# Kernel optimization log

Measured on AMD Instinct MI355X. Metric: run time of the kernel, lower is better.

Reference implementation:

```python
import jax, jax.numpy as jnp
import numpy as np

N = 100_000      # nodes
E = 1_600_000    # edges
DIN = 128
DH = 128
DOUT = 2
BN_EPS = 1e-5


def setup_inputs() -> dict:
    key = jax.random.key(0)
    ks = jax.random.split(key, 14)
    s_in = 1.0 / np.sqrt(DIN)
    s_h = 1.0 / np.sqrt(DH)
    return {
        "x": jax.random.normal(ks[0], (N, DIN), jnp.float32),
        "edge_index": jax.random.randint(ks[1], (2, E), 0, N, jnp.int32),
        "W1": jax.random.normal(ks[2], (DIN, DH), jnp.float32) * s_in,
        "b1": jnp.zeros((DH,), jnp.float32),
        "W2": jax.random.normal(ks[3], (DH, DH), jnp.float32) * s_h,
        "b2": jnp.zeros((DH,), jnp.float32),
        "W3": jax.random.normal(ks[4], (DH, DH), jnp.float32) * s_h,
        "b3": jnp.zeros((DH,), jnp.float32),
        "gamma": jnp.ones((DH,), jnp.float32),
        "beta": jnp.zeros((DH,), jnp.float32),
        "Wc": jax.random.normal(ks[5], (DH, DH), jnp.float32) * s_h,
        "bc": jnp.zeros((DH,), jnp.float32),
        "Wr": jax.random.normal(ks[6], (DH, DOUT), jnp.float32) * s_h,
        "br": jnp.zeros((DOUT,), jnp.float32),
    }


def reference(x, edge_index, W1, b1, W2, b2, W3, b3, gamma, beta, Wc, bc, Wr, br):
    src, dst = edge_index[0], edge_index[1]
    # GCN symmetric normalization with self-loops (deg includes self-loop)
    deg = jnp.zeros((N,), x.dtype).at[dst].add(1.0) + 1.0
    dinv = jax.lax.rsqrt(deg)
    coef = (dinv[src] * dinv[dst])[:, None]        # [E,1]
    self_coef = (dinv * dinv)[:, None]             # [N,1] self-loop weight

    def gcn_conv(h, W, b):
        h = h @ W                                  # [N,DH] dense transform
        agg = jnp.zeros((N, h.shape[1]), h.dtype).at[dst].add(h[src] * coef)
        return agg + h * self_coef + b

    h = jax.nn.relu(gcn_conv(x, W1, b1))
    h = jax.nn.relu(gcn_conv(h, W2, b2))   # dropout is identity at inference
    h = jax.nn.relu(gcn_conv(h, W3, b3))
    # BatchNorm1d over the node dimension (training-mode batch statistics)
    mu = h.mean(axis=0)
    var = h.var(axis=0)
    h = (h - mu) * jax.lax.rsqrt(var + BN_EPS) * gamma + beta
    h = jax.nn.relu(h @ Wc + bc)
    return h @ Wr + br
```

## Files before the change

### kernel.cpp

```cpp
#include <hip/hip_runtime.h>

#define DHC 128
#define BSHIFT 8
#define BSIZE 256

typedef __attribute__((ext_vector_type(8))) __bf16 bf16x8;
typedef __attribute__((ext_vector_type(8))) unsigned short ushort8;
typedef __attribute__((ext_vector_type(4))) float floatx4;

__device__ inline unsigned short f2bf(float f) {
    unsigned int u = __float_as_uint(f);
    return (unsigned short)((u + 0x7FFFu + ((u >> 16) & 1u)) >> 16);
}
__device__ inline float bf2f_lo(unsigned int v) { return __uint_as_float(v << 16); }
__device__ inline float bf2f_hi(unsigned int v) { return __uint_as_float(v & 0xFFFF0000u); }


__global__ __launch_bounds__(256) void bucket_hist(const int* __restrict__ dst,
                                                   int* __restrict__ bcount, int e) {
    __shared__ int h[512];
    for (int i = threadIdx.x; i < 512; i += 256) h[i] = 0;
    __syncthreads();
    int base = blockIdx.x * 4096 + threadIdx.x;
#pragma unroll
    for (int j = 0; j < 16; j++) {
        int i = base + j * 256;
        if (i < e) atomicAdd(&h[dst[i] >> BSHIFT], 1);
    }
    __syncthreads();
    for (int i = threadIdx.x; i < 512; i += 256)
        if (h[i]) atomicAdd(&bcount[i], h[i]);
}

__global__ void bucket_scan(const int* __restrict__ bcount, int* __restrict__ bbase,
                            int* __restrict__ bcur, int* __restrict__ row_ptr,
                            int nb, int n, int e) {
    __shared__ int s[512];
    int t = threadIdx.x;
    s[t] = (t < nb) ? bcount[t] : 0;
    __syncthreads();
    for (int off = 1; off < 512; off <<= 1) {
        int add = (t >= off) ? s[t - off] : 0;
        __syncthreads();
        s[t] += add;
        __syncthreads();
    }
    if (t < nb) {
        int ex = (t == 0) ? 0 : s[t - 1];
        bbase[t] = ex;
        bcur[t] = ex;
    }
    if (t == 0) {
        bbase[nb] = e;
        row_ptr[n] = e;
    }
}

__global__ __launch_bounds__(256) void bucket_scatter(const int* __restrict__ src,
                                                      const int* __restrict__ dst,
                                                      int* __restrict__ bcur,
                                                      unsigned int* __restrict__ ebuf, int e) {
    __shared__ int h[512];
    __shared__ int rsv[512];
    for (int i = threadIdx.x; i < 512; i += 256) h[i] = 0;
    __syncthreads();
    int base = blockIdx.x * 4096 + threadIdx.x;
    int sreg[16], dreg[16];
#pragma unroll
    for (int j = 0; j < 16; j++) {
        int i = base + j * 256;
        if (i < e) {
            sreg[j] = src[i];
            dreg[j] = dst[i];
            atomicAdd(&h[dreg[j] >> BSHIFT], 1);
        } else {
            dreg[j] = -1;
        }
    }
    __syncthreads();
    for (int i = threadIdx.x; i < 512; i += 256) {
        int c = h[i];
        rsv[i] = c ? atomicAdd(&bcur[i], c) : 0;
        h[i] = 0;
    }
    __syncthreads();
#pragma unroll
    for (int j = 0; j < 16; j++) {
        if (dreg[j] >= 0) {
            int b = dreg[j] >> BSHIFT;
            int pos = rsv[b] + atomicAdd(&h[b], 1);
            ebuf[pos] = (unsigned int)sreg[j] | ((unsigned int)(dreg[j] & (BSIZE - 1)) << 20);
        }
    }
}

__global__ __launch_bounds__(256) void bucket_build(const unsigned int* __restrict__ ebuf,
                                                    const int* __restrict__ bbase,
                                                    int* __restrict__ row_ptr,
                                                    int* __restrict__ csr_src,
                                                    float* __restrict__ dinv,
                                                    float* __restrict__ selfc, int n) {
    __shared__ int ldeg[256];
    __shared__ int lcur[256];
    int b = blockIdx.x;
    int t = threadIdx.x;
    int beg = bbase[b], end = bbase[b + 1];
    ldeg[t] = 0;
    __syncthreads();
    for (int i = beg + t; i < end; i += 256) atomicAdd(&ldeg[ebuf[i] >> 20], 1);
    __syncthreads();
    int deg = ldeg[t];
    lcur[t] = deg;
    __syncthreads();
    for (int off = 1; off < 256; off <<= 1) {
        int add = (t >= off) ? lcur[t - off] : 0;
        __syncthreads();
        lcur[t] += add;
        __syncthreads();
    }
    int rp = beg + lcur[t] - deg;
    int node = (b << BSHIFT) + t;
    if (node < n) {
        row_ptr[node] = rp;
        float dv = rsqrtf((float)(deg + 1));
        dinv[node] = dv;
        selfc[node] = dv * dv;
    }
    __syncthreads();
    lcur[t] = rp;
    __syncthreads();
    for (int i = beg + t; i < end; i += 256) {
        unsigned int p = ebuf[i];
        int pos = atomicAdd(&lcur[p >> 20], 1);
        csr_src[pos] = (int)(p & 0xFFFFFu);
    }
}

__global__ void wconv3_k(const float* __restrict__ W1, const float* __restrict__ W2,
                         const float* __restrict__ W3, unsigned short* __restrict__ WTall) {
    int idx = blockIdx.x * 256 + threadIdx.x;
    int wsel = idx >> 14;
    int i = idx & 16383;
    int nn = i >> 7, k = i & 127;
    const float* W = (wsel == 0) ? W1 : (wsel == 1) ? W2 : W3;
    WTall[idx] = f2bf(W[k * 128 + nn]);
}

template <int MODE, int AF32>
__global__ __launch_bounds__(256, 4) void gemm_k(const void* __restrict__ Avoid,
                                                 const unsigned short* __restrict__ WT,
                                                 const float* __restrict__ bias,
                                                 unsigned short* __restrict__ outB,
                                                 float* __restrict__ outF,
                                                 const float* __restrict__ Wr,
                                                 const float* __restrict__ br, int n) {
    __shared__ unsigned short Ws[32 * 512];
    {
        for (int c = threadIdx.x; c < 2048; c += 256) {
            int f = c >> 6;
            int l = c & 63;
            int ks = f >> 3, ct = f & 7;
            int nn = ct * 16 + (l & 15);
            int kb = ks * 32 + (l >> 4) * 8;
            *(uint4*)(&Ws[c * 8]) = *(const uint4*)(&WT[nn * 128 + kb]);
        }
    }
    __syncthreads();
    const int wave = threadIdx.x >> 6;
    const int lane = threadIdx.x & 63;
    const int rowbase = blockIdx.x * 128 + wave * 32;
    const int m = lane & 15;
    const int kq = lane >> 4;

    floatx4 acc[2][8];
#pragma unroll
    for (int rt = 0; rt < 2; rt++)
#pragma unroll
        for (int ct = 0; ct < 8; ct++) acc[rt][ct] = (floatx4){0.f, 0.f, 0.f, 0.f};

    const int r0 = min(rowbase + m, n - 1);
    const int r1 = min(rowbase + 16 + m, n - 1);

#pragma unroll
    for (int ks = 0; ks < 4; ks++) {
        const int kb = ks * 32 + kq * 8;
        bf16x8 a0, a1;
        if (AF32) {
            const float* Af = (const float*)Avoid;
            float4 f00 = *(const float4*)(Af + (size_t)r0 * 128 + kb);
            float4 f01 = *(const float4*)(Af + (size_t)r0 * 128 + kb + 4);
            float4 f10 = *(const float4*)(Af + (size_t)r1 * 128 + kb);
            float4 f11 = *(const float4*)(Af + (size_t)r1 * 128 + kb + 4);
            ushort8 u0, u1;
            u0[0] = f2bf(f00.x); u0[1] = f2bf(f00.y); u0[2] = f2bf(f00.z); u0[3] = f2bf(f00.w);
            u0[4] = f2bf(f01.x); u0[5] = f2bf(f01.y); u0[6] = f2bf(f01.z); u0[7] = f2bf(f01.w);
            u1[0] = f2bf(f10.x); u1[1] = f2bf(f10.y); u1[2] = f2bf(f10.z); u1[3] = f2bf(f10.w);
            u1[4] = f2bf(f11.x); u1[5] = f2bf(f11.y); u1[6] = f2bf(f11.z); u1[7] = f2bf(f11.w);
            a0 = __builtin_bit_cast(bf16x8, u0);
            a1 = __builtin_bit_cast(bf16x8, u1);
        } else {
            const unsigned short* Ab = (const unsigned short*)Avoid;
            a0 = __builtin_bit_cast(bf16x8, *(const ushort8*)(Ab + (size_t)r0 * 128 + kb));
            a1 = __builtin_bit_cast(bf16x8, *(const ushort8*)(Ab + (size_t)r1 * 128 + kb));
        }
#pragma unroll
        for (int ct = 0; ct < 8; ct++) {
            bf16x8 bfr = __builtin_bit_cast(bf16x8,
                *(const ushort8*)(&Ws[(ks * 8 + ct) * 512 + lane * 8]));
            acc[0][ct] = __builtin_amdgcn_mfma_f32_16x16x32_bf16(a0, bfr, acc[0][ct], 0, 0, 0);
            acc[1][ct] = __builtin_amdgcn_mfma_f32_16x16x32_bf16(a1, bfr, acc[1][ct], 0, 0, 0);
        }
    }

    if (MODE == 0) {
#pragma unroll
        for (int rt = 0; rt < 2; rt++) {
#pragma unroll
            for (int ct = 0; ct < 8; ct++) {
                int col = ct * 16 + m;
#pragma unroll
                for (int i = 0; i < 4; i++) {
                    int r = rowbase + rt * 16 + kq * 4 + i;
                    if (r < n) outB[(size_t)r * 128 + col] = f2bf(acc[rt][ct][i]);
                }
            }
        }
    } else {
        float bcv[8], wr0[8], wr1[8];
#pragma unroll
        for (int ct = 0; ct < 8; ct++) {
            int col = ct * 16 + m;
            bcv[ct] = bias[col];
            float2 wv = ((const float2*)Wr)[col];
            wr0[ct] = wv.x;
            wr1[ct] = wv.y;
        }
        float br0 = br[0], br1 = br[1];
#pragma unroll
        for (int rt = 0; rt < 2; rt++) {
#pragma unroll
            for (int i = 0; i < 4; i++) {
                float p0 = 0.f, p1 = 0.f;
#pragma unroll
                for (int ct = 0; ct < 8; ct++) {
                    float v = fmaxf(acc[rt][ct][i] + bcv[ct], 0.f);
                    p0 = fmaf(v, wr0[ct], p0);
                    p1 = fmaf(v, wr1[ct], p1);
                }
#pragma unroll
                for (int mk = 1; mk < 16; mk <<= 1) {
                    p0 += __shfl_xor(p0, mk);
                    p1 += __shfl_xor(p1, mk);
                }
                int r = rowbase + rt * 16 + kq * 4 + i;
                if (m == 0 && r < n) ((float2*)outF)[r] = make_float2(p0 + br0, p1 + br1);
            }
        }
    }
}

__global__ __launch_bounds__(256) void agg_k(const unsigned short* __restrict__ hW,
                                             const int* __restrict__ csr,
                                             const int* __restrict__ row_ptr,
                                             const float* __restrict__ dinv,
                                             const float* __restrict__ selfc,
                                             const float* __restrict__ bias,
                                             unsigned short* __restrict__ out, int n) {
    int node = blockIdx.x * 16 + (threadIdx.x >> 4);
    int t = threadIdx.x & 15;
    if (node >= n) return;
    int beg = row_ptr[node], end = row_ptr[node + 1];
    float dd = dinv[node];
    const uint4* h4 = (const uint4*)hW;
    float a[8];
#pragma unroll
    for (int i = 0; i < 8; i++) a[i] = 0.f;

    int e = beg;
    for (; e + 3 < end; e += 4) {
        int s0 = csr[e + 0], s1 = csr[e + 1], s2 = csr[e + 2], s3 = csr[e + 3];
        float c0 = dinv[s0] * dd, c1 = dinv[s1] * dd, c2 = dinv[s2] * dd, c3 = dinv[s3] * dd;
        uint4 v0 = h4[(size_t)s0 * 16 + t];
        uint4 v1 = h4[(size_t)s1 * 16 + t];
        uint4 v2 = h4[(size_t)s2 * 16 + t];
        uint4 v3 = h4[(size_t)s3 * 16 + t];
        a[0] = fmaf(c0, bf2f_lo(v0.x), a[0]); a[1] = fmaf(c0, bf2f_hi(v0.x), a[1]);
        a[2] = fmaf(c0, bf2f_lo(v0.y), a[2]); a[3] = fmaf(c0, bf2f_hi(v0.y), a[3]);
        a[4] = fmaf(c0, bf2f_lo(v0.z), a[4]); a[5] = fmaf(c0, bf2f_hi(v0.z), a[5]);
        a[6] = fmaf(c0, bf2f_lo(v0.w), a[6]); a[7] = fmaf(c0, bf2f_hi(v0.w), a[7]);
        a[0] = fmaf(c1, bf2f_lo(v1.x), a[0]); a[1] = fmaf(c1, bf2f_hi(v1.x), a[1]);
        a[2] = fmaf(c1, bf2f_lo(v1.y), a[2]); a[3] = fmaf(c1, bf2f_hi(v1.y), a[3]);
        a[4] = fmaf(c1, bf2f_lo(v1.z), a[4]); a[5] = fmaf(c1, bf2f_hi(v1.z), a[5]);
        a[6] = fmaf(c1, bf2f_lo(v1.w), a[6]); a[7] = fmaf(c1, bf2f_hi(v1.w), a[7]);
        a[0] = fmaf(c2, bf2f_lo(v2.x), a[0]); a[1] = fmaf(c2, bf2f_hi(v2.x), a[1]);
        a[2] = fmaf(c2, bf2f_lo(v2.y), a[2]); a[3] = fmaf(c2, bf2f_hi(v2.y), a[3]);
        a[4] = fmaf(c2, bf2f_lo(v2.z), a[4]); a[5] = fmaf(c2, bf2f_hi(v2.z), a[5]);
        a[6] = fmaf(c2, bf2f_lo(v2.w), a[6]); a[7] = fmaf(c2, bf2f_hi(v2.w), a[7]);
        a[0] = fmaf(c3, bf2f_lo(v3.x), a[0]); a[1] = fmaf(c3, bf2f_hi(v3.x), a[1]);
        a[2] = fmaf(c3, bf2f_lo(v3.y), a[2]); a[3] = fmaf(c3, bf2f_hi(v3.y), a[3]);
        a[4] = fmaf(c3, bf2f_lo(v3.z), a[4]); a[5] = fmaf(c3, bf2f_hi(v3.z), a[5]);
        a[6] = fmaf(c3, bf2f_lo(v3.w), a[6]); a[7] = fmaf(c3, bf2f_hi(v3.w), a[7]);
    }
    for (; e < end; e++) {
        int s = csr[e];
        float c = dinv[s] * dd;
        uint4 v = h4[(size_t)s * 16 + t];
        a[0] = fmaf(c, bf2f_lo(v.x), a[0]); a[1] = fmaf(c, bf2f_hi(v.x), a[1]);
        a[2] = fmaf(c, bf2f_lo(v.y), a[2]); a[3] = fmaf(c, bf2f_hi(v.y), a[3]);
        a[4] = fmaf(c, bf2f_lo(v.z), a[4]); a[5] = fmaf(c, bf2f_hi(v.z), a[5]);
        a[6] = fmaf(c, bf2f_lo(v.w), a[6]); a[7] = fmaf(c, bf2f_hi(v.w), a[7]);
    }

    {
        float sc = selfc[node];
        uint4 v = h4[(size_t)node * 16 + t];
        a[0] = fmaf(sc, bf2f_lo(v.x), a[0]); a[1] = fmaf(sc, bf2f_hi(v.x), a[1]);
        a[2] = fmaf(sc, bf2f_lo(v.y), a[2]); a[3] = fmaf(sc, bf2f_hi(v.y), a[3]);
        a[4] = fmaf(sc, bf2f_lo(v.z), a[4]); a[5] = fmaf(sc, bf2f_hi(v.z), a[5]);
        a[6] = fmaf(sc, bf2f_lo(v.w), a[6]); a[7] = fmaf(sc, bf2f_hi(v.w), a[7]);
    }
    float4 b0 = ((const float4*)bias)[t * 2];
    float4 b1 = ((const float4*)bias)[t * 2 + 1];
    uint4 o;
    o.x = (unsigned int)f2bf(fmaxf(a[0] + b0.x, 0.f)) |
          ((unsigned int)f2bf(fmaxf(a[1] + b0.y, 0.f)) << 16);
    o.y = (unsigned int)f2bf(fmaxf(a[2] + b0.z, 0.f)) |
          ((unsigned int)f2bf(fmaxf(a[3] + b0.w, 0.f)) << 16);
    o.z = (unsigned int)f2bf(fmaxf(a[4] + b1.x, 0.f)) |
          ((unsigned int)f2bf(fmaxf(a[5] + b1.y, 0.f)) << 16);
    o.w = (unsigned int)f2bf(fmaxf(a[6] + b1.z, 0.f)) |
          ((unsigned int)f2bf(fmaxf(a[7] + b1.w, 0.f)) << 16);
    ((uint4*)out)[(size_t)node * 16 + t] = o;
}

__global__ __launch_bounds__(256) void bn_stats(const unsigned short* __restrict__ h,
                                                float* __restrict__ gsum,
                                                float* __restrict__ gsumsq, int n) {
    __shared__ float red[4][256];
    int l = threadIdx.x & 63;
    int rs = threadIdx.x >> 6;
    float s0 = 0.f, s1 = 0.f, q0 = 0.f, q1 = 0.f;
    for (int r = blockIdx.x * 4 + rs; r < n; r += gridDim.x * 4) {
        unsigned int v = *(const unsigned int*)(h + (size_t)r * 128 + l * 2);
        float a = bf2f_lo(v), b = bf2f_hi(v);
        s0 += a;
        s1 += b;
        q0 = fmaf(a, a, q0);
        q1 = fmaf(b, b, q1);
    }
    red[0][threadIdx.x] = s0;
    red[1][threadIdx.x] = s1;
    red[2][threadIdx.x] = q0;
    red[3][threadIdx.x] = q1;
    __syncthreads();
    if (threadIdx.x < 64) {
        float S0 = 0.f, S1 = 0.f, Q0 = 0.f, Q1 = 0.f;
#pragma unroll
        for (int j = 0; j < 4; j++) {
            S0 += red[0][j * 64 + l];
            S1 += red[1][j * 64 + l];
            Q0 += red[2][j * 64 + l];
            Q1 += red[3][j * 64 + l];
        }
        atomicAdd(&gsum[2 * l + 0], S0);
        atomicAdd(&gsum[2 * l + 1], S1);
        atomicAdd(&gsumsq[2 * l + 0], Q0);
        atomicAdd(&gsumsq[2 * l + 1], Q1);
    }
}

__global__ void bn_fold(const float* __restrict__ gsum, const float* __restrict__ gsumsq,
                        const float* __restrict__ gamma, const float* __restrict__ beta,
                        const float* __restrict__ Wc, const float* __restrict__ bc,
                        unsigned short* __restrict__ WcT, float* __restrict__ bcP, float invN) {
    __shared__ float scaleS[128], shiftS[128];
    int j = threadIdx.x;
    float mu = gsum[j] * invN;
    float var = gsumsq[j] * invN - mu * mu;
    float sc = gamma[j] * rsqrtf(var + 1e-5f);
    scaleS[j] = sc;
    shiftS[j] = beta[j] - mu * sc;
    __syncthreads();
    float accB = bc[j];
    for (int k = 0; k < 128; k++) {
        float w = Wc[k * 128 + j];
        WcT[j * 128 + k] = f2bf(scaleS[k] * w);
        accB = fmaf(shiftS[k], w, accB);
    }
    bcP[j] = accB;
}


extern "C" void kernel_launch(void* const* d_in, const int* in_sizes, int n_in,
                              void* d_out, int out_size, void* d_ws, size_t ws_size,
                              hipStream_t stream) {
    const float* x = (const float*)d_in[0];
    const int* ei = (const int*)d_in[1];
    const float* W1 = (const float*)d_in[2];
    const float* b1 = (const float*)d_in[3];
    const float* W2 = (const float*)d_in[4];
    const float* b2 = (const float*)d_in[5];
    const float* W3 = (const float*)d_in[6];
    const float* b3 = (const float*)d_in[7];
    const float* gamma = (const float*)d_in[8];
    const float* beta = (const float*)d_in[9];
    const float* Wc = (const float*)d_in[10];
    const float* bc = (const float*)d_in[11];
    const float* Wr = (const float*)d_in[12];
    const float* br = (const float*)d_in[13];
    float* out = (float*)d_out;

    const int N = in_sizes[0] / DHC;
    const int E = in_sizes[1] / 2;
    const int* srcIdx = ei;
    const int* dstIdx = ei + E;
    const int NB = (N + BSIZE - 1) >> BSHIFT;

    char* w = (char*)d_ws;
    size_t off = 0;
    auto alloc = [&](size_t bytes) -> void* {
        void* p = w + off;
        off += (bytes + 255) & ~(size_t)255;
        return p;
    };
    unsigned short* bufA = (unsigned short*)alloc((size_t)N * DHC * 2);
    unsigned short* bufB = (unsigned short*)alloc((size_t)N * DHC * 2);
    unsigned int* ebuf = (unsigned int*)alloc((size_t)E * 4);
    int* csr_src = (int*)alloc((size_t)E * 4);
    int* row_ptr = (int*)alloc((size_t)(N + 1) * 4);
    float* dinv = (float*)alloc((size_t)N * 4);
    float* selfc = (float*)alloc((size_t)N * 4);
    int* bcount = (int*)alloc(512 * 4 + 256 * 4);
    float* stats = (float*)(bcount + 512);
    float* gsum = stats;
    float* gsumsq = stats + 128;
    int* bbase = (int*)alloc(512 * 4);
    int* bcur = (int*)alloc(512 * 4);
    unsigned short* WTall = (unsigned short*)alloc((size_t)3 * 16384 * 2);
    unsigned short* WT1 = WTall;
    unsigned short* WT2 = WTall + 16384;
    unsigned short* WT3 = WTall + 32768;
    unsigned short* WcT = (unsigned short*)alloc(16384 * 2);
    float* bcP = (float*)alloc(128 * 4);
    (void)ws_size; (void)n_in; (void)out_size;

    hipMemsetAsync(bcount, 0, 512 * 4 + 256 * 4, stream);

    const int EB = (E + 4095) / 4096;
    bucket_hist<<<EB, 256, 0, stream>>>(dstIdx, bcount, E);
    bucket_scan<<<1, 512, 0, stream>>>(bcount, bbase, bcur, row_ptr, NB, N, E);
    bucket_scatter<<<EB, 256, 0, stream>>>(srcIdx, dstIdx, bcur, ebuf, E);
    bucket_build<<<NB, 256, 0, stream>>>(ebuf, bbase, row_ptr, csr_src, dinv, selfc, N);

    wconv3_k<<<192, 256, 0, stream>>>(W1, W2, W3, WTall);

    const int gemmBlocks = (N + 127) / 128;
    const int aggBlocks = (N + 15) / 16;

    gemm_k<0, 1><<<gemmBlocks, 256, 0, stream>>>(x, WT1, nullptr, bufB, nullptr, nullptr, nullptr, N);
    agg_k<<<aggBlocks, 256, 0, stream>>>(bufB, csr_src, row_ptr, dinv, selfc, b1, bufA, N);
    gemm_k<0, 0><<<gemmBlocks, 256, 0, stream>>>(bufA, WT2, nullptr, bufB, nullptr, nullptr, nullptr, N);
    agg_k<<<aggBlocks, 256, 0, stream>>>(bufB, csr_src, row_ptr, dinv, selfc, b2, bufA, N);
    gemm_k<0, 0><<<gemmBlocks, 256, 0, stream>>>(bufA, WT3, nullptr, bufB, nullptr, nullptr, nullptr, N);
    agg_k<<<aggBlocks, 256, 0, stream>>>(bufB, csr_src, row_ptr, dinv, selfc, b3, bufA, N);

    bn_stats<<<256, 256, 0, stream>>>(bufA, gsum, gsumsq, N);
    bn_fold<<<1, 128, 0, stream>>>(gsum, gsumsq, gamma, beta, Wc, bc, WcT, bcP, 1.0f / (float)N);
    gemm_k<2, 0><<<gemmBlocks, 256, 0, stream>>>(bufA, WcT, bcP, nullptr, out, Wr, br, N);
}
```

Baseline: 455.8 us.

## Degree-sort aggregation nodes, fuse BN stats into last aggregation, parallelize Wc fold

```diff
diff --git a/kernel.cpp b/kernel.cpp
--- a/kernel.cpp
+++ b/kernel.cpp
@@ -98,8 +98,7 @@
                                                     const int* __restrict__ bbase,
                                                     int* __restrict__ row_ptr,
                                                     int* __restrict__ csr_src,
-                                                    float* __restrict__ dinv,
-                                                    float* __restrict__ selfc, int n) {
+                                                    float* __restrict__ dinv, int n) {
     __shared__ int ldeg[256];
     __shared__ int lcur[256];
     int b = blockIdx.x;
@@ -122,9 +121,7 @@
     int node = (b << BSHIFT) + t;
     if (node < n) {
         row_ptr[node] = rp;
-        float dv = rsqrtf((float)(deg + 1));
-        dinv[node] = dv;
-        selfc[node] = dv * dv;
+        dinv[node] = rsqrtf((float)(deg + 1));
     }
     __syncthreads();
     lcur[t] = rp;
@@ -133,6 +130,61 @@
         unsigned int p = ebuf[i];
         int pos = atomicAdd(&lcur[p >> 20], 1);
         csr_src[pos] = (int)(p & 0xFFFFFu);
+    }
+}
+
+
+__global__ __launch_bounds__(256) void deg_hist(const int* __restrict__ row_ptr,
+                                                int* __restrict__ dhist, int n) {
+    __shared__ int h[64];
+    if (threadIdx.x < 64) h[threadIdx.x] = 0;
+    __syncthreads();
+    int i = blockIdx.x * 256 + threadIdx.x;
+    if (i < n) {
+        int d = min(row_ptr[i + 1] - row_ptr[i], 63);
+        atomicAdd(&h[d], 1);
+    }
+    __syncthreads();
+    if (threadIdx.x < 64 && h[threadIdx.x]) atomicAdd(&dhist[threadIdx.x], h[threadIdx.x]);
+}
+
+__global__ void deg_scan(const int* __restrict__ dhist, int* __restrict__ dcur) {
+    __shared__ int s[64];
+    int t = threadIdx.x;
+    s[t] = dhist[t];
+    __syncthreads();
+    for (int off = 1; off < 64; off <<= 1) {
+        int add = (t >= off) ? s[t - off] : 0;
+        __syncthreads();
+        s[t] += add;
+        __syncthreads();
+    }
+    dcur[t] = (t == 0) ? 0 : s[t - 1];
+}
+
+__global__ __launch_bounds__(256) void deg_scatter(const int* __restrict__ row_ptr,
+                                                   int* __restrict__ dcur,
+                                                   int* __restrict__ order, int n) {
+    __shared__ int h[64];
+    __shared__ int rsv[64];
+    if (threadIdx.x < 64) h[threadIdx.x] = 0;
+    __syncthreads();
+    int i = blockIdx.x * 256 + threadIdx.x;
+    int d = -1;
+    if (i < n) {
+        d = min(row_ptr[i + 1] - row_ptr[i], 63);
+        atomicAdd(&h[d], 1);
+    }
+    __syncthreads();
+    if (threadIdx.x < 64) {
+        int c = h[threadIdx.x];
+        rsv[threadIdx.x] = c ? atomicAdd(&dcur[threadIdx.x], c) : 0;
+        h[threadIdx.x] = 0;
+    }
+    __syncthreads();
+    if (i < n) {
+        int p = rsv[d] + atomicAdd(&h[d], 1);
+        order[p] = i;
     }
 }
 
@@ -259,47 +311,55 @@
     }
 }
 
+template <int STATS>
 __global__ __launch_bounds__(256) void agg_k(const unsigned short* __restrict__ hW,
                                              const int* __restrict__ csr,
                                              const int* __restrict__ row_ptr,
                                              const float* __restrict__ dinv,
-                                             const float* __restrict__ selfc,
+                                             const int* __restrict__ order,
                                              const float* __restrict__ bias,
-                                             unsigned short* __restrict__ out, int n) {
-    int node = blockIdx.x * 16 + (threadIdx.x >> 4);
+                                             unsigned short* __restrict__ out,
+                                             float* __restrict__ gsum,
+                                             float* __restrict__ gsumsq, int n) {
+    __shared__ float ssum[128], ssq[128];
+    int idx = blockIdx.x * 16 + (threadIdx.x >> 4);
     int t = threadIdx.x & 15;
-    if (node >= n) return;
-    int beg = row_ptr[node], end = row_ptr[node + 1];
-    float dd = dinv[node];
+    bool valid = idx < n;
+    int node = 0, beg = 0, end = 0;
+    float dd = 0.f;
+    if (valid) {
+        node = order[idx];
+        beg = row_ptr[node];
+        end = row_ptr[node + 1];
+        dd = dinv[node];
+    }
     const uint4* h4 = (const uint4*)hW;
     float a[8];
 #pragma unroll
     for (int i = 0; i < 8; i++) a[i] = 0.f;
 
     int e = beg;
-    for (; e + 3 < end; e += 4) {
-        int s0 = csr[e + 0], s1 = csr[e + 1], s2 = csr[e + 2], s3 = csr[e + 3];
-        float c0 = dinv[s0] * dd, c1 = dinv[s1] * dd, c2 = dinv[s2] * dd, c3 = dinv[s3] * dd;
-        uint4 v0 = h4[(size_t)s0 * 16 + t];
-        uint4 v1 = h4[(size_t)s1 * 16 + t];
-        uint4 v2 = h4[(size_t)s2 * 16 + t];
-        uint4 v3 = h4[(size_t)s3 * 16 + t];
-        a[0] = fmaf(c0, bf2f_lo(v0.x), a[0]); a[1] = fmaf(c0, bf2f_hi(v0.x), a[1]);
-        a[2] = fmaf(c0, bf2f_lo(v0.y), a[2]); a[3] = fmaf(c0, bf2f_hi(v0.y), a[3]);
-        a[4] = fmaf(c0, bf2f_lo(v0.z), a[4]); a[5] = fmaf(c0, bf2f_hi(v0.z), a[5]);
-        a[6] = fmaf(c0, bf2f_lo(v0.w), a[6]); a[7] = fmaf(c0, bf2f_hi(v0.w), a[7]);
-        a[0] = fmaf(c1, bf2f_lo(v1.x), a[0]); a[1] = fmaf(c1, bf2f_hi(v1.x), a[1]);
-        a[2] = fmaf(c1, bf2f_lo(v1.y), a[2]); a[3] = fmaf(c1, bf2f_hi(v1.y), a[3]);
-        a[4] = fmaf(c1, bf2f_lo(v1.z), a[4]); a[5] = fmaf(c1, bf2f_hi(v1.z), a[5]);
-        a[6] = fmaf(c1, bf2f_lo(v1.w), a[6]); a[7] = fmaf(c1, bf2f_hi(v1.w), a[7]);
-        a[0] = fmaf(c2, bf2f_lo(v2.x), a[0]); a[1] = fmaf(c2, bf2f_hi(v2.x), a[1]);
-        a[2] = fmaf(c2, bf2f_lo(v2.y), a[2]); a[3] = fmaf(c2, bf2f_hi(v2.y), a[3]);
-        a[4] = fmaf(c2, bf2f_lo(v2.z), a[4]); a[5] = fmaf(c2, bf2f_hi(v2.z), a[5]);
-        a[6] = fmaf(c2, bf2f_lo(v2.w), a[6]); a[7] = fmaf(c2, bf2f_hi(v2.w), a[7]);
-        a[0] = fmaf(c3, bf2f_lo(v3.x), a[0]); a[1] = fmaf(c3, bf2f_hi(v3.x), a[1]);
-        a[2] = fmaf(c3, bf2f_lo(v3.y), a[2]); a[3] = fmaf(c3, bf2f_hi(v3.y), a[3]);
-        a[4] = fmaf(c3, bf2f_lo(v3.z), a[4]); a[5] = fmaf(c3, bf2f_hi(v3.z), a[5]);
-        a[6] = fmaf(c3, bf2f_lo(v3.w), a[6]); a[7] = fmaf(c3, bf2f_hi(v3.w), a[7]);
+    for (; e + 7 < end; e += 8) {
+        int s[8];
+#pragma unroll
+        for (int k = 0; k < 8; k++) s[k] = csr[e + k];
+        float c[8];
+#pragma unroll
+        for (int k = 0; k < 8; k++) c[k] = dinv[s[k]] * dd;
+        uint4 v[8];
+#pragma unroll
+        for (int k = 0; k < 8; k++) v[k] = h4[(size_t)s[k] * 16 + t];
+#pragma unroll
+        for (int k = 0; k < 8; k++) {
+            a[0] = fmaf(c[k], bf2f_lo(v[k].x), a[0]);
+            a[1] = fmaf(c[k], bf2f_hi(v[k].x), a[1]);
+            a[2] = fmaf(c[k], bf2f_lo(v[k].y), a[2]);
+            a[3] = fmaf(c[k], bf2f_hi(v[k].y), a[3]);
+            a[4] = fmaf(c[k], bf2f_lo(v[k].z), a[4]);
+            a[5] = fmaf(c[k], bf2f_hi(v[k].z), a[5]);
+            a[6] = fmaf(c[k], bf2f_lo(v[k].w), a[6]);
+            a[7] = fmaf(c[k], bf2f_hi(v[k].w), a[7]);
+        }
     }
     for (; e < end; e++) {
         int s = csr[e];
@@ -311,83 +371,86 @@
         a[6] = fmaf(c, bf2f_lo(v.w), a[6]); a[7] = fmaf(c, bf2f_hi(v.w), a[7]);
     }
 
-    {
-        float sc = selfc[node];
+    if (valid) {
+        float sc = dd * dd;
         uint4 v = h4[(size_t)node * 16 + t];
         a[0] = fmaf(sc, bf2f_lo(v.x), a[0]); a[1] = fmaf(sc, bf2f_hi(v.x), a[1]);
         a[2] = fmaf(sc, bf2f_lo(v.y), a[2]); a[3] = fmaf(sc, bf2f_hi(v.y), a[3]);
         a[4] = fmaf(sc, bf2f_lo(v.z), a[4]); a[5] = fmaf(sc, bf2f_hi(v.z), a[5]);
         a[6] = fmaf(sc, bf2f_lo(v.w), a[6]); a[7] = fmaf(sc, bf2f_hi(v.w), a[7]);
     }
+
     float4 b0 = ((const float4*)bias)[t * 2];
     float4 b1 = ((const float4*)bias)[t * 2 + 1];
-    uint4 o;
-    o.x = (unsigned int)f2bf(fmaxf(a[0] + b0.x, 0.f)) |
-          ((unsigned int)f2bf(fmaxf(a[1] + b0.y, 0.f)) << 16);
-    o.y = (unsigned int)f2bf(fmaxf(a[2] + b0.z, 0.f)) |
-          ((unsigned int)f2bf(fmaxf(a[3] + b0.w, 0.f)) << 16);
-    o.z = (unsigned int)f2bf(fmaxf(a[4] + b1.x, 0.f)) |
-          ((unsigned int)f2bf(fmaxf(a[5] + b1.y, 0.f)) << 16);
-    o.w = (unsigned int)f2bf(fmaxf(a[6] + b1.z, 0.f)) |
-          ((unsigned int)f2bf(fmaxf(a[7] + b1.w, 0.f)) << 16);
-    ((uint4*)out)[(size_t)node * 16 + t] = o;
-}
-
-__global__ __launch_bounds__(256) void bn_stats(const unsigned short* __restrict__ h,
-                                                float* __restrict__ gsum,
-                                                float* __restrict__ gsumsq, int n) {
-    __shared__ float red[4][256];
-    int l = threadIdx.x & 63;
-    int rs = threadIdx.x >> 6;
-    float s0 = 0.f, s1 = 0.f, q0 = 0.f, q1 = 0.f;
-    for (int r = blockIdx.x * 4 + rs; r < n; r += gridDim.x * 4) {
-        unsigned int v = *(const unsigned int*)(h + (size_t)r * 128 + l * 2);
-        float a = bf2f_lo(v), b = bf2f_hi(v);
-        s0 += a;
-        s1 += b;
-        q0 = fmaf(a, a, q0);
-        q1 = fmaf(b, b, q1);
-    }
-    red[0][threadIdx.x] = s0;
-    red[1][threadIdx.x] = s1;
-    red[2][threadIdx.x] = q0;
-    red[3][threadIdx.x] = q1;
-    __syncthreads();
-    if (threadIdx.x < 64) {
-        float S0 = 0.f, S1 = 0.f, Q0 = 0.f, Q1 = 0.f;
-#pragma unroll
-        for (int j = 0; j < 4; j++) {
-            S0 += red[0][j * 64 + l];
-            S1 += red[1][j * 64 + l];
-            Q0 += red[2][j * 64 + l];
-            Q1 += red[3][j * 64 + l];
-        }
-        atomicAdd(&gsum[2 * l + 0], S0);
-        atomicAdd(&gsum[2 * l + 1], S1);
-        atomicAdd(&gsumsq[2 * l + 0], Q0);
-        atomicAdd(&gsumsq[2 * l + 1], Q1);
-    }
-}
-
-__global__ void bn_fold(const float* __restrict__ gsum, const float* __restrict__ gsumsq,
-                        const float* __restrict__ gamma, const float* __restrict__ beta,
-                        const float* __restrict__ Wc, const float* __restrict__ bc,
-                        unsigned short* __restrict__ WcT, float* __restrict__ bcP, float invN) {
-    __shared__ float scaleS[128], shiftS[128];
+    float r[8];
+    r[0] = fmaxf(a[0] + b0.x, 0.f); r[1] = fmaxf(a[1] + b0.y, 0.f);
+    r[2] = fmaxf(a[2] + b0.z, 0.f); r[3] = fmaxf(a[3] + b0.w, 0.f);
+    r[4] = fmaxf(a[4] + b1.x, 0.f); r[5] = fmaxf(a[5] + b1.y, 0.f);
+    r[6] = fmaxf(a[6] + b1.z, 0.f); r[7] = fmaxf(a[7] + b1.w, 0.f);
+
+    if (valid) {
+        uint4 o;
+        o.x = (unsigned int)f2bf(r[0]) | ((unsigned int)f2bf(r[1]) << 16);
+        o.y = (unsigned int)f2bf(r[2]) | ((unsigned int)f2bf(r[3]) << 16);
+        o.z = (unsigned int)f2bf(r[4]) | ((unsigned int)f2bf(r[5]) << 16);
+        o.w = (unsigned int)f2bf(r[6]) | ((unsigned int)f2bf(r[7]) << 16);
+        ((uint4*)out)[(size_t)node * 16 + t] = o;
+    }
+
+    if (STATS) {
+        if (threadIdx.x < 128) {
+            ssum[threadIdx.x] = 0.f;
+            ssq[threadIdx.x] = 0.f;
+        }
+        __syncthreads();
+#pragma unroll
+        for (int i = 0; i < 8; i++) {
+            float sv = valid ? r[i] : 0.f;
+            float sq = sv * sv;
+            sv += __shfl_xor(sv, 16); sq += __shfl_xor(sq, 16);
+            sv += __shfl_xor(sv, 32); sq += __shfl_xor(sq, 32);
+            if ((threadIdx.x & 63) < 16) {
+                atomicAdd(&ssum[t * 8 + i], sv);
+                atomicAdd(&ssq[t * 8 + i], sq);
+            }
+        }
+        __syncthreads();
+        if (threadIdx.x < 128) {
+            atomicAdd(&gsum[threadIdx.x], ssum[threadIdx.x]);
+            atomicAdd(&gsumsq[threadIdx.x], ssq[threadIdx.x]);
+        }
+    }
+}
+
+__global__ void bn_finalize(const float* __restrict__ gsum, const float* __restrict__ gsumsq,
+                            const float* __restrict__ gamma, const float* __restrict__ beta,
+                            const float* __restrict__ bc, float* __restrict__ scale,
+                            float* __restrict__ shift, float* __restrict__ bcP, float invN) {
     int j = threadIdx.x;
     float mu = gsum[j] * invN;
     float var = gsumsq[j] * invN - mu * mu;
     float sc = gamma[j] * rsqrtf(var + 1e-5f);
-    scaleS[j] = sc;
-    shiftS[j] = beta[j] - mu * sc;
-    __syncthreads();
-    float accB = bc[j];
-    for (int k = 0; k < 128; k++) {
-        float w = Wc[k * 128 + j];
-        WcT[j * 128 + k] = f2bf(scaleS[k] * w);
-        accB = fmaf(shiftS[k], w, accB);
-    }
-    bcP[j] = accB;
+    scale[j] = sc;
+    shift[j] = beta[j] - mu * sc;
+    bcP[j] = bc[j];
+}
+
+__global__ __launch_bounds__(256) void wcfold(const float* __restrict__ Wc,
+                                              const float* __restrict__ scale,
+                                              const float* __restrict__ shift,
+                                              unsigned short* __restrict__ WcT,
+                                              float* __restrict__ bcP) {
+    __shared__ float scS[128], shS[128];
+    if (threadIdx.x < 128) {
+        scS[threadIdx.x] = scale[threadIdx.x];
+        shS[threadIdx.x] = shift[threadIdx.x];
+    }
+    __syncthreads();
+    int idx = blockIdx.x * 256 + threadIdx.x;
+    int j = idx & 127, k = idx >> 7;
+    float w = Wc[k * 128 + j];
+    WcT[j * 128 + k] = f2bf(scS[k] * w);
+    atomicAdd(&bcP[j], shS[k] * w);
 }
 
 
@@ -429,28 +492,36 @@
     int* csr_src = (int*)alloc((size_t)E * 4);
     int* row_ptr = (int*)alloc((size_t)(N + 1) * 4);
     float* dinv = (float*)alloc((size_t)N * 4);
-    float* selfc = (float*)alloc((size_t)N * 4);
-    int* bcount = (int*)alloc(512 * 4 + 256 * 4);
+    int* order = (int*)alloc((size_t)N * 4);
+    int* bcount = (int*)alloc(512 * 4 + 256 * 4 + 64 * 4);
     float* stats = (float*)(bcount + 512);
     float* gsum = stats;
     float* gsumsq = stats + 128;
+    int* dhist = (int*)(stats + 256);
     int* bbase = (int*)alloc(512 * 4);
     int* bcur = (int*)alloc(512 * 4);
+    int* dcur = (int*)alloc(64 * 4);
     unsigned short* WTall = (unsigned short*)alloc((size_t)3 * 16384 * 2);
     unsigned short* WT1 = WTall;
     unsigned short* WT2 = WTall + 16384;
     unsigned short* WT3 = WTall + 32768;
     unsigned short* WcT = (unsigned short*)alloc(16384 * 2);
+    float* scale = (float*)alloc(128 * 4);
+    float* shift = (float*)alloc(128 * 4);
     float* bcP = (float*)alloc(128 * 4);
     (void)ws_size; (void)n_in; (void)out_size;
 
-    hipMemsetAsync(bcount, 0, 512 * 4 + 256 * 4, stream);
+    hipMemsetAsync(bcount, 0, 512 * 4 + 256 * 4 + 64 * 4, stream);
 
     const int EB = (E + 4095) / 4096;
+    const int NBLK = (N + 255) / 256;
     bucket_hist<<<EB, 256, 0, stream>>>(dstIdx, bcount, E);
     bucket_scan<<<1, 512, 0, stream>>>(bcount, bbase, bcur, row_ptr, NB, N, E);
     bucket_scatter<<<EB, 256, 0, stream>>>(srcIdx, dstIdx, bcur, ebuf, E);
-    bucket_build<<<NB, 256, 0, stream>>>(ebuf, bbase, row_ptr, csr_src, dinv, selfc, N);
+    bucket_build<<<NB, 256, 0, stream>>>(ebuf, bbase, row_ptr, csr_src, dinv, N);
+    deg_hist<<<NBLK, 256, 0, stream>>>(row_ptr, dhist, N);
+    deg_scan<<<1, 64, 0, stream>>>(dhist, dcur);
+    deg_scatter<<<NBLK, 256, 0, stream>>>(row_ptr, dcur, order, N);
 
     wconv3_k<<<192, 256, 0, stream>>>(W1, W2, W3, WTall);
 
@@ -458,13 +529,13 @@
     const int aggBlocks = (N + 15) / 16;
 
     gemm_k<0, 1><<<gemmBlocks, 256, 0, stream>>>(x, WT1, nullptr, bufB, nullptr, nullptr, nullptr, N);
-    agg_k<<<aggBlocks, 256, 0, stream>>>(bufB, csr_src, row_ptr, dinv, selfc, b1, bufA, N);
+    agg_k<0><<<aggBlocks, 256, 0, stream>>>(bufB, csr_src, row_ptr, dinv, order, b1, bufA, nullptr, nullptr, N);
     gemm_k<0, 0><<<gemmBlocks, 256, 0, stream>>>(bufA, WT2, nullptr, bufB, nullptr, nullptr, nullptr, N);
-    agg_k<<<aggBlocks, 256, 0, stream>>>(bufB, csr_src, row_ptr, dinv, selfc, b2, bufA, N);
+    agg_k<0><<<aggBlocks, 256, 0, stream>>>(bufB, csr_src, row_ptr, dinv, order, b2, bufA, nullptr, nullptr, N);
     gemm_k<0, 0><<<gemmBlocks, 256, 0, stream>>>(bufA, WT3, nullptr, bufB, nullptr, nullptr, nullptr, N);
-    agg_k<<<aggBlocks, 256, 0, stream>>>(bufB, csr_src, row_ptr, dinv, selfc, b3, bufA, N);
-
-    bn_stats<<<256, 256, 0, stream>>>(bufA, gsum, gsumsq, N);
-    bn_fold<<<1, 128, 0, stream>>>(gsum, gsumsq, gamma, beta, Wc, bc, WcT, bcP, 1.0f / (float)N);
+    agg_k<1><<<aggBlocks, 256, 0, stream>>>(bufB, csr_src, row_ptr, dinv, order, b3, bufA, gsum, gsumsq, N);
+
+    bn_finalize<<<1, 128, 0, stream>>>(gsum, gsumsq, gamma, beta, bc, scale, shift, bcP, 1.0f / (float)N);
+    wcfold<<<64, 256, 0, stream>>>(Wc, scale, shift, WcT, bcP);
     gemm_k<2, 0><<<gemmBlocks, 256, 0, stream>>>(bufA, WcT, bcP, nullptr, out, Wr, br, N);
 }
```

Result: slower. 554.7 us (+21.7%).
